# Performance work log

Measured on AMD Instinct MI355X. Metric: run time of the kernel, lower is better.

Reference implementation:

```python
import jax, jax.numpy as jnp
import numpy as np

N_NODES = 100000
N_EDGES = 1600000
IN_DIM = 128
HID = 128


def setup_inputs() -> dict:
    key = jax.random.key(0)
    ks = jax.random.split(key, 12)
    s = 1.0 / np.sqrt(IN_DIM)
    sh = 1.0 / np.sqrt(HID)
    return {
        "x": jax.random.normal(ks[0], (N_NODES, IN_DIM), dtype=jnp.float32),
        "edge_index": jax.random.randint(ks[1], (2, N_EDGES), 0, N_NODES, dtype=jnp.int64),
        # SAGEConv1: lin_l (neighbors, with bias), lin_r (root, no bias)
        "W1l": jax.random.uniform(ks[2], (IN_DIM, HID), jnp.float32, -s, s),
        "b1": jax.random.uniform(ks[3], (HID,), jnp.float32, -s, s),
        "W1r": jax.random.uniform(ks[4], (IN_DIM, HID), jnp.float32, -s, s),
        # SAGEConv2
        "W2l": jax.random.uniform(ks[5], (HID, HID), jnp.float32, -sh, sh),
        "b2": jax.random.uniform(ks[6], (HID,), jnp.float32, -sh, sh),
        "W2r": jax.random.uniform(ks[7], (HID, HID), jnp.float32, -sh, sh),
        # heads
        "Wp": jax.random.uniform(ks[8], (HID, 1), jnp.float32, -sh, sh),
        "bp": jax.random.uniform(ks[9], (1,), jnp.float32, -sh, sh),
        "Wd": jax.random.uniform(ks[10], (HID, 1), jnp.float32, -sh, sh),
        "bd": jax.random.uniform(ks[11], (1,), jnp.float32, -sh, sh),
    }


def _sage_conv(x, src, dst, Wl, b, Wr, n_nodes):
    # mean aggregation over incoming edges (PyG SAGEConv default)
    msg = x[src]                                             # [E, D] gather
    agg = jax.ops.segment_sum(msg, dst, num_segments=n_nodes)  # [N, D]
    cnt = jax.ops.segment_sum(jnp.ones((src.shape[0],), x.dtype), dst,
                              num_segments=n_nodes)
    mean = agg / jnp.clip(cnt, 1.0)[:, None]
    # out = lin_l(mean_neighbors) + lin_r(x_root)
    return mean @ Wl + b + x @ Wr


def reference(x, edge_index, W1l, b1, W1r, W2l, b2, W2r, Wp, bp, Wd, bd):
    src, dst = edge_index[0], edge_index[1]
    n = x.shape[0]
    h = jax.nn.relu(_sage_conv(x, src, dst, W1l, b1, W1r, n))
    h = jax.nn.relu(_sage_conv(h, src, dst, W2l, b2, W2r, n))
    preds = h @ Wp + bp                 # [N, 1]
    diffs = jax.nn.sigmoid(h @ Wd + bd) # [N, 1]
    return (preds - diffs, preds + diffs)
```

## Files before the change

kernel.cpp:

```cpp
#include <hip/hip_runtime.h>
#include <math.h>

constexpr int NN  = 100000;
constexpr int NE  = 1600000;
constexpr int DIM = 128;
constexpr int NBUCK = (NN + 255) / 256;
constexpr int CAP  = 4608;

typedef unsigned short ushort;
typedef unsigned int uint;
typedef __attribute__((ext_vector_type(8))) short bf16x8;
typedef __attribute__((ext_vector_type(4))) float f32x4;
typedef __attribute__((ext_vector_type(4))) uint uint4v;

constexpr size_t OFF_GCUR   = 0;
constexpr size_t OFF_ROWB   = 2048;
constexpr size_t OFF_ROWE   = OFF_ROWB + 400128;
constexpr size_t OFF_COL    = OFF_ROWE + 400128;
constexpr size_t OFF_TMP    = OFF_COL  + 7206912;
constexpr size_t OFF_WT     = OFF_TMP  + 7206912;
constexpr size_t OFF_XB     = OFF_WT   + 131072;
constexpr size_t OFF_HB     = OFF_XB   + 25600000;
constexpr size_t OFF_MB     = OFF_HB   + 25600000;

__device__ __forceinline__ int eidx(const void* p, int is64, long long i) {
  return is64 ? (int)((const long long*)p)[i] : ((const int*)p)[i];
}

__device__ __forceinline__ ushort f2b(float f) {
  uint u = __float_as_uint(f);
  return (ushort)((u + 0x7FFFu + ((u >> 16) & 1u)) >> 16);
}
__device__ __forceinline__ float blo(uint u) { return __uint_as_float(u << 16); }
__device__ __forceinline__ float bhi(uint u) { return __uint_as_float(u & 0xFFFF0000u); }

__device__ __forceinline__ int detect64(const void* e) {
  __shared__ int f;
  if (threadIdx.x == 0) f = 0;
  __syncthreads();
  const uint* u = (const uint*)e;
  uint v = 0;
  for (int i = threadIdx.x; i < 4096; i += blockDim.x) v |= u[2 * i + 1];
  if (v) atomicOr(&f, 1);
  __syncthreads();
  return f == 0;
}

__global__ void k_seed(int* __restrict__ gcur) {
  int b = threadIdx.x + blockIdx.x * blockDim.x;
  if (b < NBUCK) gcur[b] = b * CAP;
}

__global__ __launch_bounds__(256) void k_bin(const void* e, int* gcur,
                                             uint* tmp) {
  __shared__ uint buf[NBUCK * 32];
  __shared__ int cnt[NBUCK];
  int is64 = detect64(e);
  for (int b = threadIdx.x; b < NBUCK; b += 256) cnt[b] = 0;
  __syncthreads();

  for (int base = blockIdx.x * 256; base < NE; base += gridDim.x * 256) {
    int i = base + threadIdx.x;
    if (i < NE) {
      int src = eidx(e, is64, i);
      int dst = eidx(e, is64, (long long)NE + i);
      int b = dst >> 8;
      uint pack = ((uint)src << 8) | (uint)(dst & 255);
      int c = atomicAdd(&cnt[b], 1);
      if (c < 32) {
        buf[b * 32 + c] = pack;
      } else {
        int p = atomicAdd(&gcur[b], 1);
        tmp[p] = pack;
      }
    }
    __syncthreads();
    for (int b = threadIdx.x; b < NBUCK; b += 256) {
      int c = min(cnt[b], 32);
      if (c >= 16) {
        int gpos = atomicAdd(&gcur[b], 16);
        uint* s = &buf[b * 32];
#pragma unroll
        for (int q = 0; q < 4; q++) {
          uint4 v = {s[q * 4 + 0], s[q * 4 + 1], s[q * 4 + 2], s[q * 4 + 3]};
          *(uint4*)(tmp + gpos + q * 4) = v;
        }
        int rem = c - 16;
        for (int q = 0; q < rem; q++) s[q] = s[16 + q];
        cnt[b] = rem;
      } else {
        cnt[b] = c;
      }
    }
    __syncthreads();
  }
  for (int b = threadIdx.x; b < NBUCK; b += 256) {
    int c = cnt[b];
    if (c > 0) {
      int gpos = atomicAdd(&gcur[b], c);
      for (int q = 0; q < c; q++) tmp[gpos + q] = buf[b * 32 + q];
    }
  }
}

__global__ __launch_bounds__(256) void k_reorder(const uint* __restrict__ tmp,
                                                 const int* __restrict__ gcur,
                                                 int* __restrict__ rowbeg,
                                                 int* __restrict__ rowend,
                                                 int* __restrict__ col) {
  __shared__ int cnt[256];
  __shared__ int lcur[256];
  __shared__ int wsum[4];
  int b = blockIdx.x;
  int t = threadIdx.x;
  int segBeg = b * CAP;
  int segEnd = gcur[b];
  cnt[t] = 0;
  __syncthreads();
  for (int j = segBeg + t; j < segEnd; j += 256)
    atomicAdd(&cnt[tmp[j] & 255], 1);
  __syncthreads();
  int c = cnt[t];
  int lane = t & 63, wid = t >> 6;
  int s = c;
#pragma unroll
  for (int off = 1; off < 64; off <<= 1) {
    int v = __shfl_up(s, off, 64);
    if (lane >= off) s += v;
  }
  if (lane == 63) wsum[wid] = s;
  __syncthreads();
  if (t == 0) {
    int r0 = wsum[0], r1 = wsum[1], r2 = wsum[2];
    wsum[1] = r0;
    wsum[2] = r0 + r1;
    wsum[3] = r0 + r1 + r2;
    wsum[0] = 0;
  }
  __syncthreads();
  int excl = s - c + wsum[wid];
  int node = (b << 8) + t;
  if (node < NN) {
    rowbeg[node] = segBeg + excl;
    rowend[node] = segBeg + excl + c;
  }
  lcur[t] = segBeg + excl;
  __syncthreads();
  for (int j = segBeg + t; j < segEnd; j += 256) {
    uint p = tmp[j];
    int pos = atomicAdd(&lcur[p & 255], 1);
    col[pos] = (int)(p >> 8);
  }
}

__global__ void k_cvtall(const float* __restrict__ x, ushort* __restrict__ xb,
                         const float* __restrict__ W1l, const float* __restrict__ W1r,
                         const float* __restrict__ W2l, const float* __restrict__ W2r,
                         ushort* __restrict__ WT) {
  int b = blockIdx.x;
  if (b < 12500) {
    int i = b * 256 + threadIdx.x;
    float4 v = ((const float4*)x)[i];
    ushort4 o = {f2b(v.x), f2b(v.y), f2b(v.z), f2b(v.w)};
    ((ushort4*)xb)[i] = o;
  } else {
    int id = (b - 12500) * 256 + threadIdx.x;
    int m = id >> 14, idx = id & 16383;
    int k = idx >> 7, n = idx & 127;
    const float* W = (m == 0) ? W1l : (m == 1) ? W1r : (m == 2) ? W2l : W2r;
    WT[m * 16384 + n * 128 + k] = f2b(W[k * 128 + n]);
  }
}

#define ACC8(P, U)                                         \
  P[0] += blo(U.x); P[1] += bhi(U.x);                      \
  P[2] += blo(U.y); P[3] += bhi(U.y);                      \
  P[4] += blo(U.z); P[5] += bhi(U.z);                      \
  P[6] += blo(U.w); P[7] += bhi(U.w);

__global__ void k_agg(const ushort* __restrict__ feat,
                      const int* __restrict__ rowbeg,
                      const int* __restrict__ rowend,
                      const int* __restrict__ col,
                      ushort* __restrict__ out) {
  int gtid = blockIdx.x * blockDim.x + threadIdx.x;
  int v = gtid >> 6;
  int lane = gtid & 63;
  if (v >= NN) return;
  int beg = rowbeg[v], end = rowend[v];
  int g = lane >> 4;
  int q = lane & 15;
  const uint4v* F4 = (const uint4v*)feat;
  float p[8] = {0.f, 0.f, 0.f, 0.f, 0.f, 0.f, 0.f, 0.f};
  int j = beg;
  for (; j + 15 < end; j += 16) {
    int c0 = __builtin_nontemporal_load(&col[j + g]);
    int c1 = __builtin_nontemporal_load(&col[j + 4 + g]);
    int c2 = __builtin_nontemporal_load(&col[j + 8 + g]);
    int c3 = __builtin_nontemporal_load(&col[j + 12 + g]);
    uint4v u0 = F4[(size_t)c0 * 16 + q];
    uint4v u1 = F4[(size_t)c1 * 16 + q];
    uint4v u2 = F4[(size_t)c2 * 16 + q];
    uint4v u3 = F4[(size_t)c3 * 16 + q];
    ACC8(p, u0)
    ACC8(p, u1)
    ACC8(p, u2)
    ACC8(p, u3)
  }
  if (j < end) {
    int last = end - 1;
    int i0 = j + g, i1 = j + 4 + g, i2 = j + 8 + g, i3 = j + 12 + g;
    int c0 = __builtin_nontemporal_load(&col[min(i0, last)]);
    int c1 = __builtin_nontemporal_load(&col[min(i1, last)]);
    int c2 = __builtin_nontemporal_load(&col[min(i2, last)]);
    int c3 = __builtin_nontemporal_load(&col[min(i3, last)]);
    uint4v u0 = F4[(size_t)c0 * 16 + q];
    uint4v u1 = F4[(size_t)c1 * 16 + q];
    uint4v u2 = F4[(size_t)c2 * 16 + q];
    uint4v u3 = F4[(size_t)c3 * 16 + q];
    uint4v z = {0, 0, 0, 0};
    if (i0 > last) u0 = z;
    if (i1 > last) u1 = z;
    if (i2 > last) u2 = z;
    if (i3 > last) u3 = z;
    ACC8(p, u0)
    ACC8(p, u1)
    ACC8(p, u2)
    ACC8(p, u3)
  }
#pragma unroll
  for (int k = 0; k < 8; k++) {
    p[k] += __shfl_xor(p[k], 16, 64);
    p[k] += __shfl_xor(p[k], 32, 64);
  }
  float inv = 1.0f / (float)max(end - beg, 1);
  if (g == 0) {
    uint4v o;
    o.x = (uint)f2b(p[0] * inv) | ((uint)f2b(p[1] * inv) << 16);
    o.y = (uint)f2b(p[2] * inv) | ((uint)f2b(p[3] * inv) << 16);
    o.z = (uint)f2b(p[4] * inv) | ((uint)f2b(p[5] * inv) << 16);
    o.w = (uint)f2b(p[6] * inv) | ((uint)f2b(p[7] * inv) << 16);
    __builtin_nontemporal_store(o, &((uint4v*)out)[(size_t)v * 16 + q]);
  }
}

template <int MODE>
__global__ __launch_bounds__(256) void k_mm(
    const ushort* __restrict__ A1, const ushort* __restrict__ A2,
    const ushort* __restrict__ B1t, const ushort* __restrict__ B2t,
    const float* __restrict__ bias, void* __restrict__ outp,
    const float* __restrict__ Wp, const float* __restrict__ bp,
    const float* __restrict__ Wd, const float* __restrict__ bd) {
  __shared__ ushort Bs[128 * 128];
  int tid = threadIdx.x;
  int wid = tid >> 6, lane = tid & 63;
  int row0 = blockIdx.x * 64 + wid * 16;
  int r = lane & 15, kg = lane >> 4;

  f32x4 acc[8];
#pragma unroll
  for (int f = 0; f < 8; f++) acc[f] = (f32x4){0.f, 0.f, 0.f, 0.f};

  int arow = row0 + r;
  bool aok = arow < NN;
  const ushort* Ar1 = A1 + (size_t)arow * DIM + kg * 8;
  const ushort* Ar2 = A2 + (size_t)arow * DIM + kg * 8;

  bf16x8 a[2][4];
#pragma unroll
  for (int ks = 0; ks < 4; ks++)
    a[0][ks] = aok ? *(const bf16x8*)(Ar1 + ks * 32)
                   : (bf16x8){0, 0, 0, 0, 0, 0, 0, 0};
#pragma unroll
  for (int ks = 0; ks < 4; ks++)
    a[1][ks] = aok ? *(const bf16x8*)(Ar2 + ks * 32)
                   : (bf16x8){0, 0, 0, 0, 0, 0, 0, 0};

#pragma unroll
  for (int half = 0; half < 2; half++) {
    const ushort* Bt = half ? B2t : B1t;
    if (half) __syncthreads();
#pragma unroll
    for (int i = 0; i < 8; i++) {
      int phys = i * 256 + tid;
      int pr = phys & 15, pkg = (phys >> 4) & 3;
      int pf = (phys >> 6) & 7, pks = (phys >> 9) & 3;
      int gchunk = (pf * 16 + pr) * 16 + pks * 4 + pkg;
      ((uint4*)Bs)[phys] = ((const uint4*)Bt)[gchunk];
    }
    __syncthreads();

#pragma unroll
    for (int ks = 0; ks < 4; ks++) {
#pragma unroll
      for (int f = 0; f < 8; f++) {
        bf16x8 b = *(const bf16x8*)&Bs[(ks * 512 + f * 64 + lane) * 8];
        acc[f] = __builtin_amdgcn_mfma_f32_16x16x32_bf16(a[half][ks], b, acc[f],
                                                         0, 0, 0);
      }
    }
  }

  if (MODE == 0) {
    ushort* O = (ushort*)outp;
#pragma unroll
    for (int rr = 0; rr < 4; rr++) {
      int orow = row0 + kg * 4 + rr;
      if (orow < NN) {
#pragma unroll
        for (int f = 0; f < 8; f++) {
          int n = f * 16 + r;
          float h = fmaxf(acc[f][rr] + bias[n], 0.f);
          O[(size_t)orow * DIM + n] = f2b(h);
        }
      }
    }
  } else {
    float* O = (float*)outp;
    float bpv = bp[0], bdv = bd[0];
#pragma unroll
    for (int rr = 0; rr < 4; rr++) {
      float p = 0.f, dv = 0.f;
#pragma unroll
      for (int f = 0; f < 8; f++) {
        int n = f * 16 + r;
        float h = fmaxf(acc[f][rr] + bias[n], 0.f);
        p += h * Wp[n];
        dv += h * Wd[n];
      }
#pragma unroll
      for (int m = 1; m < 16; m <<= 1) {
        p += __shfl_xor(p, m, 64);
        dv += __shfl_xor(dv, m, 64);
      }
      int orow = row0 + kg * 4 + rr;
      if (r == 0 && orow < NN) {
        float preds = p + bpv;
        float diffs = 1.f / (1.f + expf(-(dv + bdv)));
        O[orow] = preds - diffs;
        O[NN + orow] = preds + diffs;
      }
    }
  }
}

extern "C" void kernel_launch(void* const* d_in, const int* in_sizes, int n_in,
                              void* d_out, int out_size, void* d_ws, size_t ws_size,
                              hipStream_t stream) {
  const float* x   = (const float*)d_in[0];
  const void*  ei  = d_in[1];
  const float* W1l = (const float*)d_in[2];
  const float* b1  = (const float*)d_in[3];
  const float* W1r = (const float*)d_in[4];
  const float* W2l = (const float*)d_in[5];
  const float* b2  = (const float*)d_in[6];
  const float* W2r = (const float*)d_in[7];
  const float* Wp  = (const float*)d_in[8];
  const float* bp  = (const float*)d_in[9];
  const float* Wd  = (const float*)d_in[10];
  const float* bd  = (const float*)d_in[11];

  char* ws = (char*)d_ws;
  int* gcur   = (int*)(ws + OFF_GCUR);
  int* rowbeg = (int*)(ws + OFF_ROWB);
  int* rowend = (int*)(ws + OFF_ROWE);
  int* col    = (int*)(ws + OFF_COL);
  uint* tmp   = (uint*)(ws + OFF_TMP);
  ushort* WT  = (ushort*)(ws + OFF_WT);
  ushort* Xb  = (ushort*)(ws + OFF_XB);
  ushort* Hb  = (ushort*)(ws + OFF_HB);
  ushort* Mb  = (ushort*)(ws + OFF_MB);

  k_seed<<<1, 512, 0, stream>>>(gcur);
  k_bin<<<256, 256, 0, stream>>>(ei, gcur, tmp);
  k_reorder<<<NBUCK, 256, 0, stream>>>(tmp, gcur, rowbeg, rowend, col);

  k_cvtall<<<12756, 256, 0, stream>>>(x, Xb, W1l, W1r, W2l, W2r, WT);

  k_agg<<<(NN * 64 + 255) / 256, 256, 0, stream>>>(Xb, rowbeg, rowend, col, Mb);
  k_mm<0><<<(NN + 63) / 64, 256, 0, stream>>>(Mb, Xb, WT, WT + 16384, b1, Hb,
                                              nullptr, nullptr, nullptr, nullptr);
  k_agg<<<(NN * 64 + 255) / 256, 256, 0, stream>>>(Hb, rowbeg, rowend, col, Mb);
  k_mm<1><<<(NN + 63) / 64, 256, 0, stream>>>(Mb, Hb, WT + 32768, WT + 49152, b2,
                                              d_out, Wp, bp, Wd, bd);
}
```

Before: 256.8 us.

## Fold seed into convert kernel, finer agg tail, larger double-B-buffer matmul blocks

Folds the bucket-cursor seed kernel into the conversion kernel as an extra block, removing one launch. The aggregation tail now steps four edges at a time, then handles a masked remainder, instead of one padded 16-edge step, which avoids wasted gathers on low-degree nodes. The matmul now uses 512-thread blocks covering 128 rows and loads both weight matrices into 64KB of shared memory at once, dropping a barrier and halving the weight loads per row. The larger shared footprint and block size may reduce occupancy.

New measurement: 257.1 us. About the same (+0.1%).

```diff
diff --git a/kernel.cpp b/kernel.cpp
--- a/kernel.cpp
+++ b/kernel.cpp
@@ -44,11 +44,6 @@
   if (v) atomicOr(&f, 1);
   __syncthreads();
   return f == 0;
-}
-
-__global__ void k_seed(int* __restrict__ gcur) {
-  int b = threadIdx.x + blockIdx.x * blockDim.x;
-  if (b < NBUCK) gcur[b] = b * CAP;
 }
 
 __global__ __launch_bounds__(256) void k_bin(const void* e, int* gcur,
@@ -156,19 +151,21 @@
 __global__ void k_cvtall(const float* __restrict__ x, ushort* __restrict__ xb,
                          const float* __restrict__ W1l, const float* __restrict__ W1r,
                          const float* __restrict__ W2l, const float* __restrict__ W2r,
-                         ushort* __restrict__ WT) {
+                         ushort* __restrict__ WT, int* __restrict__ gcur) {
   int b = blockIdx.x;
   if (b < 12500) {
     int i = b * 256 + threadIdx.x;
     float4 v = ((const float4*)x)[i];
     ushort4 o = {f2b(v.x), f2b(v.y), f2b(v.z), f2b(v.w)};
     ((ushort4*)xb)[i] = o;
-  } else {
+  } else if (b < 12756) {
     int id = (b - 12500) * 256 + threadIdx.x;
     int m = id >> 14, idx = id & 16383;
     int k = idx >> 7, n = idx & 127;
     const float* W = (m == 0) ? W1l : (m == 1) ? W1r : (m == 2) ? W2l : W2r;
     WT[m * 16384 + n * 128 + k] = f2b(W[k * 128 + n]);
+  } else {
+    for (int i = threadIdx.x; i < NBUCK; i += 256) gcur[i] = i * CAP;
   }
 }
 
@@ -207,26 +204,16 @@
     ACC8(p, u2)
     ACC8(p, u3)
   }
-  if (j < end) {
-    int last = end - 1;
-    int i0 = j + g, i1 = j + 4 + g, i2 = j + 8 + g, i3 = j + 12 + g;
-    int c0 = __builtin_nontemporal_load(&col[min(i0, last)]);
-    int c1 = __builtin_nontemporal_load(&col[min(i1, last)]);
-    int c2 = __builtin_nontemporal_load(&col[min(i2, last)]);
-    int c3 = __builtin_nontemporal_load(&col[min(i3, last)]);
+  for (; j + 3 < end; j += 4) {
+    int c0 = __builtin_nontemporal_load(&col[j + g]);
     uint4v u0 = F4[(size_t)c0 * 16 + q];
-    uint4v u1 = F4[(size_t)c1 * 16 + q];
-    uint4v u2 = F4[(size_t)c2 * 16 + q];
-    uint4v u3 = F4[(size_t)c3 * 16 + q];
-    uint4v z = {0, 0, 0, 0};
-    if (i0 > last) u0 = z;
-    if (i1 > last) u1 = z;
-    if (i2 > last) u2 = z;
-    if (i3 > last) u3 = z;
     ACC8(p, u0)
-    ACC8(p, u1)
-    ACC8(p, u2)
-    ACC8(p, u3)
+  }
+  int rem = end - j;
+  if (g < rem) {
+    int c0 = __builtin_nontemporal_load(&col[j + g]);
+    uint4v u0 = F4[(size_t)c0 * 16 + q];
+    ACC8(p, u0)
   }
 #pragma unroll
   for (int k = 0; k < 8; k++) {
@@ -245,21 +232,17 @@
 }
 
 template <int MODE>
-__global__ __launch_bounds__(256) void k_mm(
+__global__ __launch_bounds__(512) void k_mm(
     const ushort* __restrict__ A1, const ushort* __restrict__ A2,
     const ushort* __restrict__ B1t, const ushort* __restrict__ B2t,
     const float* __restrict__ bias, void* __restrict__ outp,
     const float* __restrict__ Wp, const float* __restrict__ bp,
     const float* __restrict__ Wd, const float* __restrict__ bd) {
-  __shared__ ushort Bs[128 * 128];
+  __shared__ ushort Bs[2][128 * 128];
   int tid = threadIdx.x;
   int wid = tid >> 6, lane = tid & 63;
-  int row0 = blockIdx.x * 64 + wid * 16;
+  int row0 = blockIdx.x * 128 + wid * 16;
   int r = lane & 15, kg = lane >> 4;
-
-  f32x4 acc[8];
-#pragma unroll
-  for (int f = 0; f < 8; f++) acc[f] = (f32x4){0.f, 0.f, 0.f, 0.f};
 
   int arow = row0 + r;
   bool aok = arow < NN;
@@ -277,24 +260,29 @@
                    : (bf16x8){0, 0, 0, 0, 0, 0, 0, 0};
 
 #pragma unroll
+  for (int i = 0; i < 8; i++) {
+    int phys = i * 512 + tid;
+    int half = phys >> 11;
+    int ph = phys & 2047;
+    int pr = ph & 15, pkg = (ph >> 4) & 3;
+    int pf = (ph >> 6) & 7, pks = (ph >> 9) & 3;
+    int gchunk = (pf * 16 + pr) * 16 + pks * 4 + pkg;
+    const ushort* Bt = half ? B2t : B1t;
+    ((uint4*)Bs)[phys] = ((const uint4*)Bt)[gchunk];
+  }
+  __syncthreads();
+
+  f32x4 acc[8];
+#pragma unroll
+  for (int f = 0; f < 8; f++) acc[f] = (f32x4){0.f, 0.f, 0.f, 0.f};
+
+#pragma unroll
   for (int half = 0; half < 2; half++) {
-    const ushort* Bt = half ? B2t : B1t;
-    if (half) __syncthreads();
-#pragma unroll
-    for (int i = 0; i < 8; i++) {
-      int phys = i * 256 + tid;
-      int pr = phys & 15, pkg = (phys >> 4) & 3;
-      int pf = (phys >> 6) & 7, pks = (phys >> 9) & 3;
-      int gchunk = (pf * 16 + pr) * 16 + pks * 4 + pkg;
-      ((uint4*)Bs)[phys] = ((const uint4*)Bt)[gchunk];
-    }
-    __syncthreads();
-
 #pragma unroll
     for (int ks = 0; ks < 4; ks++) {
 #pragma unroll
       for (int f = 0; f < 8; f++) {
-        bf16x8 b = *(const bf16x8*)&Bs[(ks * 512 + f * 64 + lane) * 8];
+        bf16x8 b = *(const bf16x8*)&Bs[half][(ks * 512 + f * 64 + lane) * 8];
         acc[f] = __builtin_amdgcn_mfma_f32_16x16x32_bf16(a[half][ks], b, acc[f],
                                                          0, 0, 0);
       }
@@ -371,16 +359,14 @@
   ushort* Hb  = (ushort*)(ws + OFF_HB);
   ushort* Mb  = (ushort*)(ws + OFF_MB);
 
-  k_seed<<<1, 512, 0, stream>>>(gcur);
+  k_cvtall<<<12757, 256, 0, stream>>>(x, Xb, W1l, W1r, W2l, W2r, WT, gcur);
   k_bin<<<256, 256, 0, stream>>>(ei, gcur, tmp);
   k_reorder<<<NBUCK, 256, 0, stream>>>(tmp, gcur, rowbeg, rowend, col);
 
-  k_cvtall<<<12756, 256, 0, stream>>>(x, Xb, W1l, W1r, W2l, W2r, WT);
-
   k_agg<<<(NN * 64 + 255) / 256, 256, 0, stream>>>(Xb, rowbeg, rowend, col, Mb);
-  k_mm<0><<<(NN + 63) / 64, 256, 0, stream>>>(Mb, Xb, WT, WT + 16384, b1, Hb,
-                                              nullptr, nullptr, nullptr, nullptr);
+  k_mm<0><<<(NN + 127) / 128, 512, 0, stream>>>(Mb, Xb, WT, WT + 16384, b1, Hb,
+                                                nullptr, nullptr, nullptr, nullptr);
   k_agg<<<(NN * 64 + 255) / 256, 256, 0, stream>>>(Hb, rowbeg, rowend, col, Mb);
-  k_mm<1><<<(NN + 63) / 64, 256, 0, stream>>>(Mb, Hb, WT + 32768, WT + 49152, b2,
-                                              d_out, Wp, bp, Wd, bd);
-}
+  k_mm<1><<<(NN + 127) / 128, 512, 0, stream>>>(Mb, Hb, WT + 32768, WT + 49152, b2,
+                                                d_out, Wp, bp, Wd, bd);
+}
```
